# Performance work log

Measured on AMD Instinct MI355X. Metric: run time of the kernel, lower is better.

## Reference

```python
import jax, jax.numpy as jnp
import numpy as np

B, N, OBS, H, A = 8192, 8, 128, 32, 14  # batch, agents, obs dim, hx_size, actions
HID = 128  # feature MLP hidden


def setup_inputs() -> dict:
    key = jax.random.key(0)
    ks = jax.random.split(key, 24)
    f = lambda k, shp, s=0.1: (jax.random.normal(k, shp, dtype=jnp.float32) * s)
    inp = {
        'obs': f(ks[0], (B, N, OBS), 1.0),
        'hidden': f(ks[1], (B, N, H), 1.0),
        'comm': f(ks[2], (B, N, N, OBS), 1.0),
        # per-agent feature MLP: n_obs -> 128 -> 32
        'W1': f(ks[3], (N, OBS, HID)), 'b1': f(ks[4], (N, HID)),
        'W2': f(ks[5], (N, HID, H)), 'b2': f(ks[6], (N, H)),
        # per-agent comm feature MLP
        'Wc1': f(ks[7], (N, OBS, HID)), 'bc1': f(ks[8], (N, HID)),
        'Wc2': f(ks[9], (N, HID, H)), 'bc2': f(ks[10], (N, H)),
        # per-agent GRUCell(32,32): gates order r,z,n (torch: 3H x H)
        'Wih': f(ks[11], (N, H, 3 * H)), 'Whh': f(ks[12], (N, H, 3 * H)),
        'bih': f(ks[13], (N, 3 * H)), 'bhh': f(ks[14], (N, 3 * H)),
        # per-agent comm GRUCell
        'Wihc': f(ks[15], (N, H, 3 * H)), 'Whhc': f(ks[16], (N, H, 3 * H)),
        'bihc': f(ks[17], (N, 3 * H)), 'bhhc': f(ks[18], (N, 3 * H)),
        # per-agent Q head: 64 -> A
        'Wq': f(ks[19], (N, 2 * H, A)), 'bq': f(ks[20], (N, A)),
    }
    return inp


def _gru(gx, gh, h):
    # gx: [..., 3H] input gates, gh: [..., 3H] hidden gates, h: [..., H]
    xr, xz, xn = jnp.split(gx, 3, axis=-1)
    hr, hz, hn = jnp.split(gh, 3, axis=-1)
    r = jax.nn.sigmoid(xr + hr)
    z = jax.nn.sigmoid(xz + hz)
    n = jnp.tanh(xn + r * hn)
    return (1.0 - z) * n + z * h


def reference(obs, hidden, comm, W1, b1, W2, b2, Wc1, bc1, Wc2, bc2,
              Wih, Whh, bih, bhh, Wihc, Whhc, bihc, bhhc, Wq, bq):
    n = obs.shape[1]
    # per-agent feature MLP (batched over agents via einsum)
    x = jax.nn.relu(jnp.einsum('bno,noh->bnh', obs, W1) + b1)
    x = jax.nn.relu(jnp.einsum('bnh,nhk->bnk', x, W2) + b2)  # [B,N,32]
    # per-agent GRU on own feature
    gx = jnp.einsum('bnh,nhg->bng', x, Wih) + bih
    gh = jnp.einsum('bnh,nhg->bng', hidden, Whh) + bhh
    next_h = _gru(gx, gh, hidden)  # [B,N,32]
    # comm feature MLP of agent i applied to comm[:, i, j, :] for all j
    xc = jax.nn.relu(jnp.einsum('bijo,ioh->bijh', comm, Wc1) + bc1[None, :, None, :])
    xc = jax.nn.relu(jnp.einsum('bijh,ihk->bijk', xc, Wc2) + bc2[None, :, None, :])  # [B,N,N,32]
    # comm GRU of agent i, hidden broadcast over j
    gxc = jnp.einsum('bijh,ihg->bijg', xc, Wihc) + bihc[None, :, None, :]
    ghc = (jnp.einsum('bih,ihg->big', hidden, Whhc) + bhhc)[:, :, None, :]
    hc = _gru(gxc, ghc, hidden[:, :, None, :])  # [B,N,N,32]
    # mean over j != i
    mask = (1.0 - jnp.eye(n, dtype=hc.dtype))[None, :, :, None]
    comm_values = (hc * mask).sum(axis=2) / (n - 1)  # [B,N,32]
    # per-agent Q head on concat
    feat = jnp.concatenate([next_h, comm_values], axis=-1)  # [B,N,64]
    q = jnp.einsum('bnf,nfa->bna', feat, Wq) + bq  # [B,N,A]
    return q, next_h
```

## Files before the change

kernel.cpp:

```cpp
#include <hip/hip_runtime.h>
#include <cstdint>
#include <cstddef>

#define B_    8192
#define N_    8
#define OBS_  128
#define HID_  128
#define H_    32
#define G3_   96
#define A_    14
#define QSIZE (B_*N_*A_)

#define TPB   256
#define GRIDX 32

#define K1_W1   0
#define K1_W2   16384
#define K1_WIH  20480
#define K1_B1   23552
#define K1_B2   23680
#define K1_BIH  23712
#define K1_BHH  23808
#define K1_IN   23904
#define K1_XH   32352
#define K1_NF   36576
#define K1_BYTES (K1_NF*4)

#define K2_WC1  0
#define K2_WC2  16384
#define K2_WIHC 20480
#define K2_WQ   23552
#define K2_BC1  24448
#define K2_BC2  24576
#define K2_BIHC 24608
#define K2_BHHC 24704
#define K2_BQ   24800
#define K2_IN   24816
#define K2_H2   33264
#define K2_HID  35568
#define K2_GHC  35824
#define K2_CV   36592
#define K2_NF   36848
#define K2_BYTES (K2_NF*4)

__device__ __forceinline__ float sigf(float x) { return 1.0f/(1.0f + __expf(-x)); }
__device__ __forceinline__ float tanh_fast(float x) {
  x = fminf(15.0f, fmaxf(-15.0f, x));
  const float e = __expf(2.0f*x);
  return (e - 1.0f)/(e + 1.0f);
}
__device__ __forceinline__ float relu_(float x){ return fmaxf(x, 0.0f); }

__global__ void __launch_bounds__(TPB)
qnet_own(const float* __restrict__ obs, const float* __restrict__ hidden,
         const float* __restrict__ W1, const float* __restrict__ b1,
         const float* __restrict__ W2, const float* __restrict__ b2,
         const float* __restrict__ Wih, const float* __restrict__ Whh,
         const float* __restrict__ bih, const float* __restrict__ bhh,
         float* __restrict__ nh_out)
{
  extern __shared__ float sm[];
  const int tid = threadIdx.x;
  const int n   = blockIdx.y;
  const int cg  = tid & 15;
  const int rg  = tid >> 4;

  {
    const float4* w1g = (const float4*)(W1 + (size_t)n*OBS_*HID_);
    float4* w1s = (float4*)(sm + K1_W1);
    for (int l = tid; l < 4096; l += TPB) w1s[l] = w1g[l];
    const float4* w2g = (const float4*)(W2 + (size_t)n*HID_*H_);
    float4* w2s = (float4*)(sm + K1_W2);
    for (int l = tid; l < 1024; l += TPB) w2s[l] = w2g[l];
    const float4* wig = (const float4*)(Wih + (size_t)n*H_*G3_);
    float4* wis = (float4*)(sm + K1_WIH);
    for (int l = tid; l < 768; l += TPB) wis[l] = wig[l];
    if (tid < 32) ((float4*)(sm+K1_B1))[tid] = ((const float4*)(b1 + n*HID_))[tid];
    if (tid >= 64 && tid < 72)   ((float4*)(sm+K1_B2 ))[tid-64 ] = ((const float4*)(b2  + n*H_ ))[tid-64 ];
    if (tid >= 96 && tid < 120)  ((float4*)(sm+K1_BIH))[tid-96 ] = ((const float4*)(bih + n*G3_))[tid-96 ];
    if (tid >= 128 && tid < 152) ((float4*)(sm+K1_BHH))[tid-128] = ((const float4*)(bhh + n*G3_))[tid-128];
  }
  __syncthreads();

  for (int t = 0; t < B_/(64*GRIDX); ++t) {
    const int b0 = (t*GRIDX + (int)blockIdx.x) * 64;

    for (int l = tid; l < 2048; l += TPB) {
      const int r = l >> 5, c = l & 31;
      const float4 v = ((const float4*)(obs + ((size_t)(b0+r)*N_ + n)*OBS_))[c];
      *(float4*)(sm + K1_IN + r*132 + 4*c) = v;
    }
    for (int l = tid; l < 1024; l += TPB) {
      const int r = l >> 4, c = l & 15;
      const float2 v = ((const float2*)(hidden + ((size_t)(b0+r)*N_ + n)*H_))[c];
      *(float2*)(sm + K1_XH + r*66 + 32 + 2*c) = v;
    }
    __syncthreads();

    float acc[4][8];
    {
      const float4 bA = *(const float4*)(sm + K1_B1 + 4*cg);
      const float4 bB = *(const float4*)(sm + K1_B1 + 64 + 4*cg);
#pragma unroll
      for (int q = 0; q < 4; ++q) {
        acc[q][0]=bA.x; acc[q][1]=bA.y; acc[q][2]=bA.z; acc[q][3]=bA.w;
        acc[q][4]=bB.x; acc[q][5]=bB.y; acc[q][6]=bB.z; acc[q][7]=bB.w;
      }
      const float* wb = sm + K1_W1 + 4*cg;
#pragma unroll 4
      for (int k = 0; k < 128; ++k) {
        const float4 w0 = *(const float4*)(wb + k*128);
        const float4 w1 = *(const float4*)(wb + k*128 + 64);
#pragma unroll
        for (int q = 0; q < 4; ++q) {
          const float a = sm[K1_IN + (4*rg+q)*132 + k];
          acc[q][0] = fmaf(a, w0.x, acc[q][0]);
          acc[q][1] = fmaf(a, w0.y, acc[q][1]);
          acc[q][2] = fmaf(a, w0.z, acc[q][2]);
          acc[q][3] = fmaf(a, w0.w, acc[q][3]);
          acc[q][4] = fmaf(a, w1.x, acc[q][4]);
          acc[q][5] = fmaf(a, w1.y, acc[q][5]);
          acc[q][6] = fmaf(a, w1.z, acc[q][6]);
          acc[q][7] = fmaf(a, w1.w, acc[q][7]);
        }
      }
    }
    __syncthreads();
#pragma unroll
    for (int q = 0; q < 4; ++q) {
      *(float4*)(sm + K1_IN + (4*rg+q)*132 + 4*cg) =
        make_float4(relu_(acc[q][0]),relu_(acc[q][1]),relu_(acc[q][2]),relu_(acc[q][3]));
      *(float4*)(sm + K1_IN + (4*rg+q)*132 + 64 + 4*cg) =
        make_float4(relu_(acc[q][4]),relu_(acc[q][5]),relu_(acc[q][6]),relu_(acc[q][7]));
    }
    __syncthreads();

    {
      float a2[4][2];
      const float2 b2v = *(const float2*)(sm + K1_B2 + 2*cg);
#pragma unroll
      for (int q = 0; q < 4; ++q) { a2[q][0]=b2v.x; a2[q][1]=b2v.y; }
      const float* wb = sm + K1_W2 + 2*cg;
#pragma unroll 4
      for (int k = 0; k < 128; ++k) {
        const float2 w = *(const float2*)(wb + k*32);
#pragma unroll
        for (int q = 0; q < 4; ++q) {
          const float a = sm[K1_IN + (4*rg+q)*132 + k];
          a2[q][0] = fmaf(a, w.x, a2[q][0]);
          a2[q][1] = fmaf(a, w.y, a2[q][1]);
        }
      }
#pragma unroll
      for (int q = 0; q < 4; ++q)
        *(float2*)(sm + K1_XH + (4*rg+q)*66 + 2*cg) =
          make_float2(relu_(a2[q][0]), relu_(a2[q][1]));
    }
    __syncthreads();

    {
      float ag[4][6];
#pragma unroll
      for (int q = 0; q < 4; ++q)
#pragma unroll
        for (int c = 0; c < 6; ++c) ag[q][c] = sm[K1_BIH + 6*cg + c];
      const float* wb = sm + K1_WIH + 6*cg;
#pragma unroll 2
      for (int k = 0; k < 32; ++k) {
        const float2 wA = *(const float2*)(wb + k*96);
        const float2 wB = *(const float2*)(wb + k*96 + 2);
        const float2 wC = *(const float2*)(wb + k*96 + 4);
#pragma unroll
        for (int q = 0; q < 4; ++q) {
          const float a = sm[K1_XH + (4*rg+q)*66 + k];
          ag[q][0]=fmaf(a,wA.x,ag[q][0]); ag[q][1]=fmaf(a,wA.y,ag[q][1]);
          ag[q][2]=fmaf(a,wB.x,ag[q][2]); ag[q][3]=fmaf(a,wB.y,ag[q][3]);
          ag[q][4]=fmaf(a,wC.x,ag[q][4]); ag[q][5]=fmaf(a,wC.y,ag[q][5]);
        }
      }
#pragma unroll
      for (int q = 0; q < 4; ++q) {
        *(float2*)(sm + K1_IN + (4*rg+q)*100 + 6*cg)     = make_float2(ag[q][0], ag[q][1]);
        *(float2*)(sm + K1_IN + (4*rg+q)*100 + 6*cg + 2) = make_float2(ag[q][2], ag[q][3]);
        *(float2*)(sm + K1_IN + (4*rg+q)*100 + 6*cg + 4) = make_float2(ag[q][4], ag[q][5]);
      }
    }

    float gh[4][6];
#pragma unroll
    for (int q = 0; q < 4; ++q) {
      gh[q][0]=sm[K1_BHH + 2*cg];      gh[q][1]=sm[K1_BHH + 2*cg + 1];
      gh[q][2]=sm[K1_BHH + 32 + 2*cg]; gh[q][3]=sm[K1_BHH + 32 + 2*cg + 1];
      gh[q][4]=sm[K1_BHH + 64 + 2*cg]; gh[q][5]=sm[K1_BHH + 64 + 2*cg + 1];
    }
    {
      const float* whg = Whh + (size_t)n*H_*G3_ + 2*cg;
#pragma unroll 2
      for (int k = 0; k < 32; ++k) {
        const float2 wr = *(const float2*)(whg + k*96);
        const float2 wz = *(const float2*)(whg + k*96 + 32);
        const float2 wn = *(const float2*)(whg + k*96 + 64);
#pragma unroll
        for (int q = 0; q < 4; ++q) {
          const float a = sm[K1_XH + (4*rg+q)*66 + 32 + k];
          gh[q][0]=fmaf(a,wr.x,gh[q][0]); gh[q][1]=fmaf(a,wr.y,gh[q][1]);
          gh[q][2]=fmaf(a,wz.x,gh[q][2]); gh[q][3]=fmaf(a,wz.y,gh[q][3]);
          gh[q][4]=fmaf(a,wn.x,gh[q][4]); gh[q][5]=fmaf(a,wn.y,gh[q][5]);
        }
      }
    }
    __syncthreads();

#pragma unroll
    for (int q = 0; q < 4; ++q) {
      const float* g = sm + K1_IN + (4*rg+q)*100;
      float o[2];
#pragma unroll
      for (int c = 0; c < 2; ++c) {
        const int h = 2*cg + c;
        const float r  = sigf(g[h]    + gh[q][0+c]);
        const float z  = sigf(g[32+h] + gh[q][2+c]);
        const float nn = tanh_fast(fmaf(r, gh[q][4+c], g[64+h]));
        const float hp = sm[K1_XH + (4*rg+q)*66 + 32 + h];
        o[c] = fmaf(z, hp - nn, nn);
      }
      *(float2*)(nh_out + ((size_t)(b0 + 4*rg+q)*N_ + n)*H_ + 2*cg) = make_float2(o[0], o[1]);
    }
    __syncthreads();
  }
}

__global__ void __launch_bounds__(TPB)
qnet_comm(const float* __restrict__ comm, const float* __restrict__ hidden,
          const float* __restrict__ Wc1, const float* __restrict__ bc1,
          const float* __restrict__ Wc2, const float* __restrict__ bc2,
          const float* __restrict__ Wihc, const float* __restrict__ bihc,
          const float* __restrict__ bhhc, const float* __restrict__ Whhc,
          const float* __restrict__ Wq, const float* __restrict__ bq,
          const float* __restrict__ nh_in, float* __restrict__ q_out)
{
  extern __shared__ float sm[];
  const int tid = threadIdx.x;
  const int i   = blockIdx.y;
  const int cg  = tid & 15;
  const int rg  = tid >> 4;

  {
    const float4* g1 = (const float4*)(Wc1 + (size_t)i*OBS_*HID_);
    float4* s1 = (float4*)(sm + K2_WC1);
    for (int l = tid; l < 4096; l += TPB) s1[l] = g1[l];
    const float4* g2 = (const float4*)(Wc2 + (size_t)i*HID_*H_);
    float4* s2 = (float4*)(sm + K2_WC2);
    for (int l = tid; l < 1024; l += TPB) s2[l] = g2[l];
    const float4* g3 = (const float4*)(Wihc + (size_t)i*H_*G3_);
    float4* s3 = (float4*)(sm + K2_WIHC);
    for (int l = tid; l < 768; l += TPB) s3[l] = g3[l];
    const float4* g4 = (const float4*)(Wq + (size_t)i*2*H_*A_);
    float4* s4 = (float4*)(sm + K2_WQ);
    for (int l = tid; l < 224; l += TPB) s4[l] = g4[l];
    if (tid < 32) ((float4*)(sm+K2_BC1))[tid] = ((const float4*)(bc1 + i*OBS_))[tid];
    if (tid >= 64 && tid < 72)   ((float4*)(sm+K2_BC2 ))[tid-64 ] = ((const float4*)(bc2  + i*H_ ))[tid-64 ];
    if (tid >= 96 && tid < 120)  ((float4*)(sm+K2_BIHC))[tid-96 ] = ((const float4*)(bihc + i*G3_))[tid-96 ];
    if (tid >= 128 && tid < 152) ((float4*)(sm+K2_BHHC))[tid-128] = ((const float4*)(bhhc + i*G3_))[tid-128];
    if (tid >= 160 && tid < 174) sm[K2_BQ + tid-160] = bq[i*A_ + tid-160];
  }
  __syncthreads();

  for (int t = 0; t < B_/(8*GRIDX); ++t) {
    const int b0 = (t*GRIDX + (int)blockIdx.x) * 8;

    for (int l = tid; l < 2048; l += TPB) {
      const int r = l >> 5, c = l & 31;
      const size_t grow = (size_t)(b0 + (r>>3))*64 + (size_t)i*8 + (r&7);
      const float4 v = ((const float4*)(comm + grow*OBS_))[c];
      *(float4*)(sm + K2_IN + r*132 + 4*c) = v;
    }
    if (tid < 64) {
      const int bb = tid >> 3, c = tid & 7;
      const float4 v = ((const float4*)(hidden + ((size_t)(b0+bb)*N_ + i)*H_))[c];
      *(float4*)(sm + K2_HID + bb*32 + 4*c) = v;
    }
    __syncthreads();

    float acc[4][8];
    {
      const float4 bA = *(const float4*)(sm + K2_BC1 + 4*cg);
      const float4 bB = *(const float4*)(sm + K2_BC1 + 64 + 4*cg);
#pragma unroll
      for (int q = 0; q < 4; ++q) {
        acc[q][0]=bA.x; acc[q][1]=bA.y; acc[q][2]=bA.z; acc[q][3]=bA.w;
        acc[q][4]=bB.x; acc[q][5]=bB.y; acc[q][6]=bB.z; acc[q][7]=bB.w;
      }
      const float* wb = sm + K2_WC1 + 4*cg;
#pragma unroll 4
      for (int k = 0; k < 128; ++k) {
        const float4 w0 = *(const float4*)(wb + k*128);
        const float4 w1 = *(const float4*)(wb + k*128 + 64);
#pragma unroll
        for (int q = 0; q < 4; ++q) {
          const float a = sm[K2_IN + (4*rg+q)*132 + k];
          acc[q][0] = fmaf(a, w0.x, acc[q][0]);
          acc[q][1] = fmaf(a, w0.y, acc[q][1]);
          acc[q][2] = fmaf(a, w0.z, acc[q][2]);
          acc[q][3] = fmaf(a, w0.w, acc[q][3]);
          acc[q][4] = fmaf(a, w1.x, acc[q][4]);
          acc[q][5] = fmaf(a, w1.y, acc[q][5]);
          acc[q][6] = fmaf(a, w1.z, acc[q][6]);
          acc[q][7] = fmaf(a, w1.w, acc[q][7]);
        }
      }
    }
    __syncthreads();
#pragma unroll
    for (int q = 0; q < 4; ++q) {
      *(float4*)(sm + K2_IN + (4*rg+q)*132 + 4*cg) =
        make_float4(relu_(acc[q][0]),relu_(acc[q][1]),relu_(acc[q][2]),relu_(acc[q][3]));
      *(float4*)(sm + K2_IN + (4*rg+q)*132 + 64 + 4*cg) =
        make_float4(relu_(acc[q][4]),relu_(acc[q][5]),relu_(acc[q][6]),relu_(acc[q][7]));
    }
    __syncthreads();

    {
      float a2[4][2];
      const float2 b2v = *(const float2*)(sm + K2_BC2 + 2*cg);
#pragma unroll
      for (int q = 0; q < 4; ++q) { a2[q][0]=b2v.x; a2[q][1]=b2v.y; }
      const float* wb = sm + K2_WC2 + 2*cg;
#pragma unroll 4
      for (int k = 0; k < 128; ++k) {
        const float2 w = *(const float2*)(wb + k*32);
#pragma unroll
        for (int q = 0; q < 4; ++q) {
          const float a = sm[K2_IN + (4*rg+q)*132 + k];
          a2[q][0] = fmaf(a, w.x, a2[q][0]);
          a2[q][1] = fmaf(a, w.y, a2[q][1]);
        }
      }
#pragma unroll
      for (int q = 0; q < 4; ++q)
        *(float2*)(sm + K2_H2 + (4*rg+q)*36 + 2*cg) =
          make_float2(relu_(a2[q][0]), relu_(a2[q][1]));
    }
    __syncthreads();

    {
      float ag[4][6];
#pragma unroll
      for (int q = 0; q < 4; ++q)
#pragma unroll
        for (int c = 0; c < 6; ++c) ag[q][c] = sm[K2_BIHC + 6*cg + c];
      const float* wb = sm + K2_WIHC + 6*cg;
#pragma unroll 2
      for (int k = 0; k < 32; ++k) {
        const float2 wA = *(const float2*)(wb + k*96);
        const float2 wB = *(const float2*)(wb + k*96 + 2);
        const float2 wC = *(const float2*)(wb + k*96 + 4);
#pragma unroll
        for (int q = 0; q < 4; ++q) {
          const float a = sm[K2_H2 + (4*rg+q)*36 + k];
          ag[q][0]=fmaf(a,wA.x,ag[q][0]); ag[q][1]=fmaf(a,wA.y,ag[q][1]);
          ag[q][2]=fmaf(a,wB.x,ag[q][2]); ag[q][3]=fmaf(a,wB.y,ag[q][3]);
          ag[q][4]=fmaf(a,wC.x,ag[q][4]); ag[q][5]=fmaf(a,wC.y,ag[q][5]);
        }
      }
#pragma unroll
      for (int q = 0; q < 4; ++q) {
        *(float2*)(sm + K2_IN + (4*rg+q)*100 + 6*cg)     = make_float2(ag[q][0], ag[q][1]);
        *(float2*)(sm + K2_IN + (4*rg+q)*100 + 6*cg + 2) = make_float2(ag[q][2], ag[q][3]);
        *(float2*)(sm + K2_IN + (4*rg+q)*100 + 6*cg + 4) = make_float2(ag[q][4], ag[q][5]);
      }
    }
    {
      const int bb = tid >> 5;
      const int g0 = 3*(tid & 31);
      float g3v[3] = { sm[K2_BHHC+g0], sm[K2_BHHC+g0+1], sm[K2_BHHC+g0+2] };
      const float* wh = Whhc + (size_t)i*H_*G3_ + g0;
#pragma unroll 4
      for (int k = 0; k < 32; ++k) {
        const float hv = sm[K2_HID + bb*32 + k];
        g3v[0] = fmaf(hv, wh[k*96+0], g3v[0]);
        g3v[1] = fmaf(hv, wh[k*96+1], g3v[1]);
        g3v[2] = fmaf(hv, wh[k*96+2], g3v[2]);
      }
      sm[K2_GHC + bb*96 + g0]   = g3v[0];
      sm[K2_GHC + bb*96 + g0+1] = g3v[1];
      sm[K2_GHC + bb*96 + g0+2] = g3v[2];
    }
    __syncthreads();

    {
      const int bb = tid >> 5, h = tid & 31;
      const float hp = sm[K2_HID + bb*32 + h];
      const float hr = sm[K2_GHC + bb*96 + h];
      const float hz = sm[K2_GHC + bb*96 + 32 + h];
      const float hn = sm[K2_GHC + bb*96 + 64 + h];
      float s = 0.0f;
#pragma unroll
      for (int j = 0; j < 8; ++j) {
        const float* g = sm + K2_IN + (bb*8 + j)*100;
        const float r  = sigf(g[h]    + hr);
        const float z  = sigf(g[32+h] + hz);
        const float nn = tanh_fast(fmaf(r, hn, g[64+h]));
        const float hc = fmaf(z, hp - nn, nn);
        s += (j == i) ? 0.0f : hc;
      }
      sm[K2_CV + tid] = s * (1.0f/7.0f);
    }
    __syncthreads();

    if (tid < 112) {
      const int bb = tid / 14, a = tid - bb*14;
      const float* nh = nh_in + ((size_t)(b0+bb)*N_ + i)*H_;
      float qv = sm[K2_BQ + a];
#pragma unroll 4
      for (int h = 0; h < 32; ++h)
        qv = fmaf(nh[h], sm[K2_WQ + h*A_ + a], qv);
#pragma unroll 4
      for (int h = 0; h < 32; ++h)
        qv = fmaf(sm[K2_CV + bb*32 + h], sm[K2_WQ + (32+h)*A_ + a], qv);
      q_out[((size_t)(b0+bb)*N_ + i)*A_ + a] = qv;
    }
  }
}

extern "C" void kernel_launch(void* const* d_in, const int* in_sizes, int n_in,
                              void* d_out, int out_size, void* d_ws, size_t ws_size,
                              hipStream_t stream) {
  const float* obs    = (const float*)d_in[0];
  const float* hidden = (const float*)d_in[1];
  const float* comm   = (const float*)d_in[2];
  const float* W1  = (const float*)d_in[3];  const float* b1  = (const float*)d_in[4];
  const float* W2  = (const float*)d_in[5];  const float* b2  = (const float*)d_in[6];
  const float* Wc1 = (const float*)d_in[7];  const float* bc1 = (const float*)d_in[8];
  const float* Wc2 = (const float*)d_in[9];  const float* bc2 = (const float*)d_in[10];
  const float* Wih = (const float*)d_in[11]; const float* Whh = (const float*)d_in[12];
  const float* bih = (const float*)d_in[13]; const float* bhh = (const float*)d_in[14];
  const float* Wihc= (const float*)d_in[15]; const float* Whhc= (const float*)d_in[16];
  const float* bihc= (const float*)d_in[17]; const float* bhhc= (const float*)d_in[18];
  const float* Wq  = (const float*)d_in[19]; const float* bq  = (const float*)d_in[20];

  float* q_out  = (float*)d_out;
  float* nh_out = q_out + QSIZE;

  (void)hipFuncSetAttribute(reinterpret_cast<const void*>(qnet_own),
                            hipFuncAttributeMaxDynamicSharedMemorySize, K1_BYTES);
  (void)hipFuncSetAttribute(reinterpret_cast<const void*>(qnet_comm),
                            hipFuncAttributeMaxDynamicSharedMemorySize, K2_BYTES);

  dim3 blk(TPB);
  qnet_own <<<dim3(GRIDX, N_), blk, K1_BYTES, stream>>>(
      obs, hidden, W1, b1, W2, b2, Wih, Whh, bih, bhh, nh_out);
  qnet_comm<<<dim3(GRIDX, N_), blk, K2_BYTES, stream>>>(
      comm, hidden, Wc1, bc1, Wc2, bc2, Wihc, bihc, bhhc, Whhc, Wq, bq,
      nh_out, q_out);
}
```

Baseline: 1.233 ms.

## Read weights from global/L2 instead of LDS and quadruple grid size

Stops staging the per-agent weight matrices in shared memory and reads them directly from global memory, relying on cache hits, which shrinks LDS per block from about 147KB to about 50KB. It also raises the grid from 32 to 128 blocks per agent and adds a minimum of 3 blocks per CU to launch bounds, aiming for more resident waves and less per-block weight-load prologue. In exchange, every inner-loop weight access becomes a global/L1 load instead of an LDS read, which could raise latency if caching is poor.

```diff
diff --git a/kernel.cpp b/kernel.cpp
--- a/kernel.cpp
+++ b/kernel.cpp
@@ -12,35 +12,28 @@
 #define QSIZE (B_*N_*A_)
 
 #define TPB   256
-#define GRIDX 32
-
-#define K1_W1   0
-#define K1_W2   16384
-#define K1_WIH  20480
-#define K1_B1   23552
-#define K1_B2   23680
-#define K1_BIH  23712
-#define K1_BHH  23808
-#define K1_IN   23904
-#define K1_XH   32352
-#define K1_NF   36576
+#define GRIDX 128
+
+#define K1_B1   0
+#define K1_B2   128
+#define K1_BIH  160
+#define K1_BHH  256
+#define K1_IN   352
+#define K1_XH   8800
+#define K1_NF   13024
 #define K1_BYTES (K1_NF*4)
 
-#define K2_WC1  0
-#define K2_WC2  16384
-#define K2_WIHC 20480
-#define K2_WQ   23552
-#define K2_BC1  24448
-#define K2_BC2  24576
-#define K2_BIHC 24608
-#define K2_BHHC 24704
-#define K2_BQ   24800
-#define K2_IN   24816
-#define K2_H2   33264
-#define K2_HID  35568
-#define K2_GHC  35824
-#define K2_CV   36592
-#define K2_NF   36848
+#define K2_BC1  0
+#define K2_BC2  128
+#define K2_BIHC 160
+#define K2_BHHC 256
+#define K2_BQ   352
+#define K2_IN   368
+#define K2_H2   8816
+#define K2_HID  11120
+#define K2_GHC  11376
+#define K2_CV   12144
+#define K2_NF   12400
 #define K2_BYTES (K2_NF*4)
 
 __device__ __forceinline__ float sigf(float x) { return 1.0f/(1.0f + __expf(-x)); }
@@ -51,7 +44,7 @@
 }
 __device__ __forceinline__ float relu_(float x){ return fmaxf(x, 0.0f); }
 
-__global__ void __launch_bounds__(TPB)
+__global__ void __launch_bounds__(TPB, 3)
 qnet_own(const float* __restrict__ obs, const float* __restrict__ hidden,
          const float* __restrict__ W1, const float* __restrict__ b1,
          const float* __restrict__ W2, const float* __restrict__ b2,
@@ -65,21 +58,15 @@
   const int cg  = tid & 15;
   const int rg  = tid >> 4;
 
-  {
-    const float4* w1g = (const float4*)(W1 + (size_t)n*OBS_*HID_);
-    float4* w1s = (float4*)(sm + K1_W1);
-    for (int l = tid; l < 4096; l += TPB) w1s[l] = w1g[l];
-    const float4* w2g = (const float4*)(W2 + (size_t)n*HID_*H_);
-    float4* w2s = (float4*)(sm + K1_W2);
-    for (int l = tid; l < 1024; l += TPB) w2s[l] = w2g[l];
-    const float4* wig = (const float4*)(Wih + (size_t)n*H_*G3_);
-    float4* wis = (float4*)(sm + K1_WIH);
-    for (int l = tid; l < 768; l += TPB) wis[l] = wig[l];
-    if (tid < 32) ((float4*)(sm+K1_B1))[tid] = ((const float4*)(b1 + n*HID_))[tid];
-    if (tid >= 64 && tid < 72)   ((float4*)(sm+K1_B2 ))[tid-64 ] = ((const float4*)(b2  + n*H_ ))[tid-64 ];
-    if (tid >= 96 && tid < 120)  ((float4*)(sm+K1_BIH))[tid-96 ] = ((const float4*)(bih + n*G3_))[tid-96 ];
-    if (tid >= 128 && tid < 152) ((float4*)(sm+K1_BHH))[tid-128] = ((const float4*)(bhh + n*G3_))[tid-128];
-  }
+  const float* W1g  = W1  + (size_t)n*OBS_*HID_;
+  const float* W2g  = W2  + (size_t)n*HID_*H_;
+  const float* Wihg = Wih + (size_t)n*H_*G3_;
+  const float* Whhg = Whh + (size_t)n*H_*G3_;
+
+  if (tid < 32)       ((float4*)(sm+K1_B1 ))[tid]    = ((const float4*)(b1  + n*HID_))[tid];
+  else if (tid < 40)  ((float4*)(sm+K1_B2 ))[tid-32] = ((const float4*)(b2  + n*H_ ))[tid-32];
+  else if (tid < 64)  ((float4*)(sm+K1_BIH))[tid-40] = ((const float4*)(bih + n*G3_))[tid-40];
+  else if (tid < 88)  ((float4*)(sm+K1_BHH))[tid-64] = ((const float4*)(bhh + n*G3_))[tid-64];
   __syncthreads();
 
   for (int t = 0; t < B_/(64*GRIDX); ++t) {
@@ -106,7 +93,7 @@
         acc[q][0]=bA.x; acc[q][1]=bA.y; acc[q][2]=bA.z; acc[q][3]=bA.w;
         acc[q][4]=bB.x; acc[q][5]=bB.y; acc[q][6]=bB.z; acc[q][7]=bB.w;
       }
-      const float* wb = sm + K1_W1 + 4*cg;
+      const float* wb = W1g + 4*cg;
 #pragma unroll 4
       for (int k = 0; k < 128; ++k) {
         const float4 w0 = *(const float4*)(wb + k*128);
@@ -140,7 +127,7 @@
       const float2 b2v = *(const float2*)(sm + K1_B2 + 2*cg);
 #pragma unroll
       for (int q = 0; q < 4; ++q) { a2[q][0]=b2v.x; a2[q][1]=b2v.y; }
-      const float* wb = sm + K1_W2 + 2*cg;
+      const float* wb = W2g + 2*cg;
 #pragma unroll 4
       for (int k = 0; k < 128; ++k) {
         const float2 w = *(const float2*)(wb + k*32);
@@ -164,7 +151,7 @@
       for (int q = 0; q < 4; ++q)
 #pragma unroll
         for (int c = 0; c < 6; ++c) ag[q][c] = sm[K1_BIH + 6*cg + c];
-      const float* wb = sm + K1_WIH + 6*cg;
+      const float* wb = Wihg + 6*cg;
 #pragma unroll 2
       for (int k = 0; k < 32; ++k) {
         const float2 wA = *(const float2*)(wb + k*96);
@@ -194,7 +181,7 @@
       gh[q][4]=sm[K1_BHH + 64 + 2*cg]; gh[q][5]=sm[K1_BHH + 64 + 2*cg + 1];
     }
     {
-      const float* whg = Whh + (size_t)n*H_*G3_ + 2*cg;
+      const float* whg = Whhg + 2*cg;
 #pragma unroll 2
       for (int k = 0; k < 32; ++k) {
         const float2 wr = *(const float2*)(whg + k*96);
@@ -230,7 +217,7 @@
   }
 }
 
-__global__ void __launch_bounds__(TPB)
+__global__ void __launch_bounds__(TPB, 3)
 qnet_comm(const float* __restrict__ comm, const float* __restrict__ hidden,
           const float* __restrict__ Wc1, const float* __restrict__ bc1,
           const float* __restrict__ Wc2, const float* __restrict__ bc2,
@@ -245,25 +232,17 @@
   const int cg  = tid & 15;
   const int rg  = tid >> 4;
 
-  {
-    const float4* g1 = (const float4*)(Wc1 + (size_t)i*OBS_*HID_);
-    float4* s1 = (float4*)(sm + K2_WC1);
-    for (int l = tid; l < 4096; l += TPB) s1[l] = g1[l];
-    const float4* g2 = (const float4*)(Wc2 + (size_t)i*HID_*H_);
-    float4* s2 = (float4*)(sm + K2_WC2);
-    for (int l = tid; l < 1024; l += TPB) s2[l] = g2[l];
-    const float4* g3 = (const float4*)(Wihc + (size_t)i*H_*G3_);
-    float4* s3 = (float4*)(sm + K2_WIHC);
-    for (int l = tid; l < 768; l += TPB) s3[l] = g3[l];
-    const float4* g4 = (const float4*)(Wq + (size_t)i*2*H_*A_);
-    float4* s4 = (float4*)(sm + K2_WQ);
-    for (int l = tid; l < 224; l += TPB) s4[l] = g4[l];
-    if (tid < 32) ((float4*)(sm+K2_BC1))[tid] = ((const float4*)(bc1 + i*OBS_))[tid];
-    if (tid >= 64 && tid < 72)   ((float4*)(sm+K2_BC2 ))[tid-64 ] = ((const float4*)(bc2  + i*H_ ))[tid-64 ];
-    if (tid >= 96 && tid < 120)  ((float4*)(sm+K2_BIHC))[tid-96 ] = ((const float4*)(bihc + i*G3_))[tid-96 ];
-    if (tid >= 128 && tid < 152) ((float4*)(sm+K2_BHHC))[tid-128] = ((const float4*)(bhhc + i*G3_))[tid-128];
-    if (tid >= 160 && tid < 174) sm[K2_BQ + tid-160] = bq[i*A_ + tid-160];
-  }
+  const float* Wc1g  = Wc1  + (size_t)i*OBS_*HID_;
+  const float* Wc2g  = Wc2  + (size_t)i*HID_*H_;
+  const float* Wihcg = Wihc + (size_t)i*H_*G3_;
+  const float* Whhcg = Whhc + (size_t)i*H_*G3_;
+  const float* Wqg   = Wq   + (size_t)i*2*H_*A_;
+
+  if (tid < 32)        ((float4*)(sm+K2_BC1 ))[tid]    = ((const float4*)(bc1  + i*OBS_))[tid];
+  else if (tid < 40)   ((float4*)(sm+K2_BC2 ))[tid-32] = ((const float4*)(bc2  + i*H_ ))[tid-32];
+  else if (tid < 64)   ((float4*)(sm+K2_BIHC))[tid-40] = ((const float4*)(bihc + i*G3_))[tid-40];
+  else if (tid < 88)   ((float4*)(sm+K2_BHHC))[tid-64] = ((const float4*)(bhhc + i*G3_))[tid-64];
+  else if (tid < 102)  sm[K2_BQ + tid-88] = bq[i*A_ + tid-88];
   __syncthreads();
 
   for (int t = 0; t < B_/(8*GRIDX); ++t) {
@@ -291,7 +270,7 @@
         acc[q][0]=bA.x; acc[q][1]=bA.y; acc[q][2]=bA.z; acc[q][3]=bA.w;
         acc[q][4]=bB.x; acc[q][5]=bB.y; acc[q][6]=bB.z; acc[q][7]=bB.w;
       }
-      const float* wb = sm + K2_WC1 + 4*cg;
+      const float* wb = Wc1g + 4*cg;
 #pragma unroll 4
       for (int k = 0; k < 128; ++k) {
         const float4 w0 = *(const float4*)(wb + k*128);
@@ -325,7 +304,7 @@
       const float2 b2v = *(const float2*)(sm + K2_BC2 + 2*cg);
 #pragma unroll
       for (int q = 0; q < 4; ++q) { a2[q][0]=b2v.x; a2[q][1]=b2v.y; }
-      const float* wb = sm + K2_WC2 + 2*cg;
+      const float* wb = Wc2g + 2*cg;
 #pragma unroll 4
       for (int k = 0; k < 128; ++k) {
         const float2 w = *(const float2*)(wb + k*32);
@@ -349,7 +328,7 @@
       for (int q = 0; q < 4; ++q)
 #pragma unroll
         for (int c = 0; c < 6; ++c) ag[q][c] = sm[K2_BIHC + 6*cg + c];
-      const float* wb = sm + K2_WIHC + 6*cg;
+      const float* wb = Wihcg + 6*cg;
 #pragma unroll 2
       for (int k = 0; k < 32; ++k) {
         const float2 wA = *(const float2*)(wb + k*96);
@@ -374,7 +353,7 @@
       const int bb = tid >> 5;
       const int g0 = 3*(tid & 31);
       float g3v[3] = { sm[K2_BHHC+g0], sm[K2_BHHC+g0+1], sm[K2_BHHC+g0+2] };
-      const float* wh = Whhc + (size_t)i*H_*G3_ + g0;
+      const float* wh = Whhcg + g0;
 #pragma unroll 4
       for (int k = 0; k < 32; ++k) {
         const float hv = sm[K2_HID + bb*32 + k];
@@ -414,10 +393,10 @@
       float qv = sm[K2_BQ + a];
 #pragma unroll 4
       for (int h = 0; h < 32; ++h)
-        qv = fmaf(nh[h], sm[K2_WQ + h*A_ + a], qv);
+        qv = fmaf(nh[h], Wqg[h*A_ + a], qv);
 #pragma unroll 4
       for (int h = 0; h < 32; ++h)
-        qv = fmaf(sm[K2_CV + bb*32 + h], sm[K2_WQ + (32+h)*A_ + a], qv);
+        qv = fmaf(sm[K2_CV + bb*32 + h], Wqg[(32+h)*A_ + a], qv);
       q_out[((size_t)(b0+bb)*N_ + i)*A_ + a] = qv;
     }
   }
@@ -442,11 +421,6 @@
   float* q_out  = (float*)d_out;
   float* nh_out = q_out + QSIZE;
 
-  (void)hipFuncSetAttribute(reinterpret_cast<const void*>(qnet_own),
-                            hipFuncAttributeMaxDynamicSharedMemorySize, K1_BYTES);
-  (void)hipFuncSetAttribute(reinterpret_cast<const void*>(qnet_comm),
-                            hipFuncAttributeMaxDynamicSharedMemorySize, K2_BYTES);
-
   dim3 blk(TPB);
   qnet_own <<<dim3(GRIDX, N_), blk, K1_BYTES, stream>>>(
       obs, hidden, W1, b1, W2, b2, Wih, Whh, bih, bhh, nh_out);
```

Result: slower. 1.274 ms (+3.3%).
